# Optimization experiments

Measured on AMD Instinct MI355X. Metric: run time of the kernel, lower is better.

The kernel has to match this reference:

```python
import jax, jax.numpy as jnp
import numpy as np

# Model constants (match init_kwargs)
V_SIZE = 6144
D = 1024
K = 32            # SNN frames per token
N_LAYERS = 4
B = 2
S = 256
SUR_ALPHA = 4.0   # surrogate sigmoid alpha (dynamic _mpd_alpha affects grads only; fixed here)


def rmsnorm(x, w, eps=1e-6):
    return x * jax.lax.rsqrt(jnp.mean(x * x, axis=-1, keepdims=True) + eps) * w


def plif_scan(beta, u, v_th, alpha_sur):
    """PLIF row-param parallel scan: V[t] = beta*V[t-1] + u[t] (v_init = 0),
    spike[t] = Heaviside(V[t] - v_th) with sigmoid surrogate (straight-through).
    u: (T, B, D); beta, v_th: broadcastable to (B, D)."""
    A = jnp.broadcast_to(beta, u.shape)

    def comb(c1, c2):
        a1, b1 = c1
        a2, b2 = c2
        return a1 * a2, a2 * b1 + b2

    _, V = jax.lax.associative_scan(comb, (A, u))  # linear first-order recurrence
    vs = V - v_th
    sg = jax.nn.sigmoid(alpha_sur * vs)
    spike = jax.lax.stop_gradient((vs >= 0).astype(u.dtype) - sg) + sg
    return spike


def setup_inputs() -> dict:
    key = jax.random.key(0)
    ks = jax.random.split(key, 8)
    sc = 1.0 / np.sqrt(D)
    inp = {}
    inp["token_ids"] = jax.random.randint(ks[0], (B, S), 0, V_SIZE)
    inp["embed"] = jax.random.normal(ks[1], (V_SIZE, D), jnp.float32) * 0.02
    inp["W_in"] = jax.random.normal(ks[2], (N_LAYERS, D, D), jnp.float32) * sc
    inp["W_out"] = jax.random.normal(ks[3], (N_LAYERS, D, D), jnp.float32) * sc
    inp["layer_beta"] = jnp.full((N_LAYERS, D), 0.5, jnp.float32)  # tau=2 -> decay 0.5
    inp["layer_vth"] = jnp.full((N_LAYERS, D), 0.3, jnp.float32)
    inp["out_norm_w"] = jnp.ones((D,), jnp.float32)
    inp["out_beta"] = jnp.full((D,), 0.5, jnp.float32)
    inp["out_vth"] = jnp.full((D,), 0.3, jnp.float32)
    inp["out_alpha"] = jnp.ones((1,), jnp.float32)
    inp["decode_w"] = jax.random.normal(ks[4], (D, D), jnp.float32) * sc
    inp["decode_b"] = jnp.zeros((D,), jnp.float32)
    inp["li_norm_w"] = jnp.ones((D,), jnp.float32)
    return inp


def reference(token_ids, embed, W_in, W_out, layer_beta, layer_vth,
              out_norm_w, out_beta, out_vth, out_alpha,
              decode_w, decode_b, li_norm_w):
    b, s = token_ids.shape
    # encode: embed lookup, repeat each token K times -> (T=s*K, b, D)
    emb = embed[token_ids]                                   # (b, s, D)
    x = jnp.repeat(emb[:, :, None, :], K, axis=2)            # (b, s, K, D)
    x = x.reshape(b, s * K, D).transpose(1, 0, 2)            # (T, b, D)
    # SNN decoder layers (PLIF recurrence + residual projections)
    for i in range(N_LAYERS):
        u = jnp.einsum('tbd,de->tbe', x, W_in[i])
        spike = plif_scan(layer_beta[i], u, layer_vth[i], SUR_ALPHA)
        x = x + jnp.einsum('tbd,de->tbe', spike * layer_vth[i], W_out[i])
    # decode: RMSNorm -> output PLIF neuron parallel scan -> spike current
    h = rmsnorm(x, out_norm_w)
    spike = plif_scan(out_beta, out_alpha * h, out_vth, SUR_ALPHA)
    v_out = spike * out_vth                                  # spike_current_activation
    # K-frame aggregation: (T, b, D) -> (s, K, b, D) -> mean over K -> (b, s, D)
    decoded = v_out.reshape(s, K, b, D).mean(axis=1).transpose(1, 0, 2)
    h2 = decoded @ decode_w.T + decode_b                     # decode_proj
    h2 = rmsnorm(h2, li_norm_w)                              # LateralInhibition norm
    return h2 @ embed.T                                      # tied LM head -> (b, s, V)
```

## Files before the change

### kernel.cpp

```cpp
#include <hip/hip_runtime.h>

typedef __bf16 bf16x8 __attribute__((ext_vector_type(8)));
typedef __bf16 bf16x4 __attribute__((ext_vector_type(4)));
typedef __bf16 bf16x2 __attribute__((ext_vector_type(2)));
typedef float  f32x4  __attribute__((ext_vector_type(4)));

constexpr int Bc = 2, Sc = 256, Kc = 32, Tc = 8192, Dc = 1024, Vc = 6144, NLc = 4;
constexpr int NPANEL = (Tc * Bc) / 128;
constexpr int UTS = NLc * Dc;

__device__ __forceinline__ void gload16(const void* g, void* l) {
    __builtin_amdgcn_global_load_lds(
        (const __attribute__((address_space(1))) unsigned int*)g,
        (__attribute__((address_space(3))) unsigned int*)l,
        16, 0, 0);
}

__device__ __forceinline__ int xcd_swz(int lin, int nwg) {
    int q = nwg >> 3, r = nwg & 7;
    int x = lin & 7, o = lin >> 3;
    int base = (x < r) ? x * (q + 1) : r * (q + 1) + (x - r) * q;
    return base + o;
}

__device__ __forceinline__ bool gate_or(const int* f, int n, int p) {
    bool g = false;
    for (int j = 0; j < n; ++j) g = g || (f[j * NPANEL + p] != 0);
    return g;
}

template<int EPI, int BM, int BN>
__global__ __launch_bounds__(256)
void gemm_bt(const __bf16* __restrict__ A, const __bf16* __restrict__ BT,
             int M, int N, int Kd,
             float* __restrict__ Cout, __bf16* __restrict__ outb,
             const float* __restrict__ bias)
{
    constexpr int MI = BM / 32, NI = BN / 32;
    constexpr int CA = BM / 32, CB = BN / 32;
    __shared__ char lds[(BM + BN) * 128];
    char* As = lds;
    char* Bs = lds + BM * 128;
    const int tid  = threadIdx.x;
    const int lane = tid & 63;
    const int wid  = tid >> 6;
    const int wm   = wid & 1, wn = wid >> 1;

    const int nwg = gridDim.x * gridDim.y;
    const int lin = blockIdx.y * gridDim.x + blockIdx.x;
    const int swz = xcd_swz(lin, nwg);
    const int bn  = (swz % gridDim.x) * BN;
    const int bm  = (swz / gridDim.x) * BM;

    const __bf16* asrc[CA];
#pragma unroll
    for (int i = 0; i < CA; ++i) {
        int chunk = i * 256 + tid;
        int row = chunk >> 3, kc = chunk & 7;
        int kcs = kc ^ (row & 7);
        asrc[i] = A + (size_t)(bm + row) * Kd + kcs * 8;
    }
    const __bf16* bsrc[CB];
#pragma unroll
    for (int i = 0; i < CB; ++i) {
        int chunk = i * 256 + tid;
        int row = chunk >> 3, kc = chunk & 7;
        int kcs = kc ^ (row & 7);
        bsrc[i] = BT + (size_t)(bn + row) * Kd + kcs * 8;
    }

    f32x4 acc[MI][NI] = {};

    for (int kt = 0; kt < Kd; kt += 64) {
#pragma unroll
        for (int i = 0; i < CA; ++i)
            gload16(asrc[i] + kt, As + (i * 256 + tid) * 16);
#pragma unroll
        for (int i = 0; i < CB; ++i)
            gload16(bsrc[i] + kt, Bs + (i * 256 + tid) * 16);
        __syncthreads();
#pragma unroll
        for (int kk = 0; kk < 2; ++kk) {
            const int ko = kk * 64 + ((lane >> 4) << 4);
            bf16x8 af[MI], bfr[NI];
#pragma unroll
            for (int mi = 0; mi < MI; ++mi) {
                int row = wm * (BM / 2) + mi * 16 + (lane & 15);
                af[mi] = *(const bf16x8*)(As + row * 128 + (ko ^ ((row & 7) << 4)));
            }
#pragma unroll
            for (int ni = 0; ni < NI; ++ni) {
                int row = wn * (BN / 2) + ni * 16 + (lane & 15);
                bfr[ni] = *(const bf16x8*)(Bs + row * 128 + (ko ^ ((row & 7) << 4)));
            }
#pragma unroll
            for (int mi = 0; mi < MI; ++mi)
#pragma unroll
                for (int ni = 0; ni < NI; ++ni)
                    acc[mi][ni] = __builtin_amdgcn_mfma_f32_16x16x32_bf16(
                        af[mi], bfr[ni], acc[mi][ni], 0, 0, 0);
        }
        __syncthreads();
    }

    const int cc = lane & 15, cr = (lane >> 4) * 4;
#pragma unroll
    for (int mi = 0; mi < MI; ++mi) {
#pragma unroll
        for (int ni = 0; ni < NI; ++ni) {
            int gcol = bn + wn * (BN / 2) + ni * 16 + cc;
#pragma unroll
            for (int r = 0; r < 4; ++r) {
                int grow = bm + wm * (BM / 2) + mi * 16 + cr + r;
                size_t idx = (size_t)grow * N + gcol;
                float v = acc[mi][ni][r];
                if (EPI == 0)      Cout[idx] = v;
                else if (EPI == 2) Cout[idx] = v + bias[gcol];
                else               outb[idx] = (__bf16)v;
            }
        }
    }
}

__global__ __launch_bounds__(1024)
void fused_layer(const __bf16* __restrict__ utok, const float* __restrict__ Win,
                 const float* __restrict__ Wout, const float* __restrict__ beta,
                 const float* __restrict__ vth, const __bf16* __restrict__ dxR,
                 __bf16* __restrict__ dxW, int* __restrict__ flags_all, int l)
{
    const int e  = threadIdx.x;
    const int p  = blockIdx.x;
    const int t0 = p * 64;
    const float bet = beta[e], vt = vth[e];
    float a = bet, S = 1.0f;
#pragma unroll
    for (int i = 0; i < 5; ++i) { S = S * (1.0f + a); a = a * a; }
    int* flags_l = flags_all + l * NPANEL;

    __shared__ int fm;
    __shared__ __bf16 srow[Dc];
    if (e == 0) fm = 0;
    __syncthreads();

    const bool pd  = gate_or(flags_all, l, p);
    const bool pdw = (p > 0) && gate_or(flags_all, l, p - 1);

    auto ut = [&](int tk, int b) -> float {
        return (float)utok[((size_t)tk * Bc + b) * UTS + e];
    };
    auto du_at = [&](int t, int b) -> float {
        __syncthreads();
        srow[e] = dxR[((size_t)t * Bc + b) * Dc + e];
        __syncthreads();
        float acc = 0.f;
        for (int d = 0; d < Dc; ++d)
            acc = fmaf((float)srow[d], Win[(size_t)d * Dc + e], acc);
        return acc;
    };

    bool spike = false;
    for (int b = 0; b < Bc; ++b) {
        float V = 0.f;
        if (p > 0) {
            if (!pdw) {
                for (int ti = 0; ti < 2; ++ti)
                    V = fmaf(a, V, ut(2 * p - 2 + ti, b) * S);
            } else {
                for (int t = t0 - 64; t < t0; ++t)
                    V = fmaf(bet, V, ut(t >> 5, b) + du_at(t, b));
            }
        }
        if (!pd) {
            for (int ti = 0; ti < 2; ++ti) {
                const float u = ut(2 * p + ti, b);
                float V1 = fmaf(bet, V, u);
                V = fmaf(a, V, u * S);
                spike = spike || (fmaxf(V1, V) >= vt);
            }
        } else {
            for (int k = 0; k < 64; ++k) {
                const int t = t0 + k;
                V = fmaf(bet, V, ut(t >> 5, b) + du_at(t, b));
                spike = spike || (V >= vt);
            }
        }
    }
    if (__any(spike) && (e & 63) == 0) atomicOr(&fm, 1);
    __syncthreads();
    const bool f = (fm != 0);
    if (e == 0) flags_l[p] = f ? 1 : 0;
    if (!f) {
        if (pd) {
            for (int rr = 0; rr < 128; ++rr)
                dxW[(size_t)(t0 * Bc + rr) * Dc + e] =
                    dxR[(size_t)(t0 * Bc + rr) * Dc + e];
        }
        return;
    }

    const __bf16 vtb = (__bf16)vt, zb = (__bf16)0.f;
    for (int b = 0; b < Bc; ++b) {
        float V = 0.f;
        if (p > 0) {
            if (!pdw) {
                for (int ti = 0; ti < 2; ++ti)
                    V = fmaf(a, V, ut(2 * p - 2 + ti, b) * S);
            } else {
                for (int t = t0 - 64; t < t0; ++t)
                    V = fmaf(bet, V, ut(t >> 5, b) + du_at(t, b));
            }
        }
        for (int k = 0; k < 64; ++k) {
            const int t = t0 + k;
            float u = ut(t >> 5, b);
            if (pd) u += du_at(t, b);
            V = fmaf(bet, V, u);
            __syncthreads();
            srow[e] = (V >= vt) ? vtb : zb;
            __syncthreads();
            float acc2 = 0.f;
            for (int d = 0; d < Dc; ++d)
                acc2 = fmaf((float)srow[d], Wout[(size_t)d * Dc + e], acc2);
            size_t r = (size_t)t * Bc + b;
            float base = pd ? (float)dxR[r * Dc + e] : 0.f;
            dxW[r * Dc + e] = (__bf16)(base + acc2);
        }
    }
}

__global__ __launch_bounds__(256)
void out_scan2(const float* __restrict__ htok, const __bf16* __restrict__ dxf,
               const int* __restrict__ tok, const float* __restrict__ embed,
               const float* __restrict__ onw, const float* __restrict__ alpha_p,
               const float* __restrict__ obeta, const float* __restrict__ ovth,
               const int* __restrict__ flags, __bf16* __restrict__ decoded)
{
    const int tid = threadIdx.x;
    const int s = blockIdx.x, b = blockIdx.y;
    const float al = alpha_p[0];
    const f32x4 bet = ((const f32x4*)obeta)[tid];
    const f32x4 vt  = ((const f32x4*)ovth)[tid];
    f32x4 a = bet, S = {1.f, 1.f, 1.f, 1.f};
#pragma unroll
    for (int i = 0; i < 5; ++i) {
#pragma unroll
        for (int c = 0; c < 4; ++c) { S[c] *= 1.0f + a[c]; a[c] *= a[c]; }
    }

    const int t0 = s * Kc;
    const int tlo = (t0 >= 64) ? t0 - 64 : 0;
    bool dirty = false;
    for (int c = tlo >> 6; c <= (t0 + Kc - 1) >> 6; ++c)
        dirty = dirty || gate_or(flags, NLc, c);

    f32x4 V = {0,0,0,0}, sum = {0,0,0,0};
    if (!dirty) {
        for (int tk = (s >= 2 ? s - 2 : 0); tk < s; ++tk) {
            f32x4 h = ((const f32x4*)(htok + ((size_t)tk * Bc + b) * Dc))[tid];
#pragma unroll
            for (int c = 0; c < 4; ++c) V[c] = fmaf(a[c], V[c], al * h[c] * S[c]);
        }
        f32x4 h = ((const f32x4*)(htok + ((size_t)s * Bc + b) * Dc))[tid];
        for (int k = 0; k < Kc; ++k) {
#pragma unroll
            for (int c = 0; c < 4; ++c) {
                V[c] = fmaf(bet[c], V[c], al * h[c]);
                sum[c] += (V[c] >= vt[c]) ? vt[c] : 0.f;
            }
        }
    } else {
        const f32x4 wv = ((const f32x4*)onw)[tid];
        __shared__ float red[4];
        for (int t = tlo; t < t0 + Kc; ++t) {
            const bool g = gate_or(flags, NLc, t >> 6);
            f32x4 h;
            if (g) {
                size_t r = (size_t)t * Bc + b;
                int id = tok[b * Sc + (t >> 5)];
                f32x4 v = ((const f32x4*)(embed + (size_t)id * Dc))[tid];
                bf16x4 dv = ((const bf16x4*)(dxf + r * Dc))[tid];
#pragma unroll
                for (int c = 0; c < 4; ++c) v[c] += (float)dv[c];
                float ss = v[0]*v[0] + v[1]*v[1] + v[2]*v[2] + v[3]*v[3];
#pragma unroll
                for (int off = 32; off >= 1; off >>= 1) ss += __shfl_down(ss, off);
                if ((tid & 63) == 0) red[tid >> 6] = ss;
                __syncthreads();
                float tot = red[0] + red[1] + red[2] + red[3];
                __syncthreads();
                float sc = rsqrtf(tot * (1.0f / Dc) + 1e-6f);
#pragma unroll
                for (int c = 0; c < 4; ++c) h[c] = v[c] * sc * wv[c];
            } else {
                h = ((const f32x4*)(htok + ((size_t)(t >> 5) * Bc + b) * Dc))[tid];
            }
#pragma unroll
            for (int c = 0; c < 4; ++c) {
                V[c] = fmaf(bet[c], V[c], al * h[c]);
                if (t >= t0) sum[c] += (V[c] >= vt[c]) ? vt[c] : 0.f;
            }
        }
    }
    bf16x4 o;
#pragma unroll
    for (int c = 0; c < 4; ++c) o[c] = (__bf16)(sum[c] * (1.0f / 32.0f));
    ((bf16x4*)(decoded + ((size_t)b * Sc + s) * Dc))[tid] = o;
}

__global__ __launch_bounds__(256)
void prep(const float* __restrict__ W_in, const float* __restrict__ embed,
          const float* __restrict__ decode_w, const int* __restrict__ tok,
          const float* __restrict__ onw, __bf16* __restrict__ wT_in,
          __bf16* __restrict__ emb_bf, __bf16* __restrict__ decw_bf,
          __bf16* __restrict__ xtok, float* __restrict__ h_tok,
          int* __restrict__ flags)
{
    const int blk = blockIdx.x;
    const int tid = threadIdx.x;
    if (blk < 4096) {
        __shared__ float tile[32][33];
        const int mat = blk >> 10;
        const int t2  = blk & 1023;
        const int d0  = (t2 & 31) * 32, e0 = (t2 >> 5) * 32;
        const float* Wm = W_in + (size_t)mat * Dc * Dc;
        __bf16*      Wo = wT_in + (size_t)mat * Dc * Dc;
        const int tx = tid & 31, ty = tid >> 5;
#pragma unroll
        for (int i = 0; i < 4; ++i)
            tile[ty + i*8][tx] = Wm[(size_t)(d0 + ty + i*8) * Dc + e0 + tx];
        __syncthreads();
        const int txp = tid & 15, tyw = tid >> 4;
#pragma unroll
        for (int i = 0; i < 2; ++i) {
            int r = tyw + 16 * i;
            bf16x2 o;
            o[0] = (__bf16)tile[2*txp][r];
            o[1] = (__bf16)tile[2*txp + 1][r];
            *(bf16x2*)(&Wo[(size_t)(e0 + r) * Dc + d0 + 2*txp]) = o;
        }
    } else if (blk < 7680) {
        const float* src; __bf16* dst; int idx;
        if (blk < 7168) { src = embed;    dst = emb_bf;  idx = (blk - 4096) * 256 + tid; }
        else            { src = decode_w; dst = decw_bf; idx = (blk - 7168) * 256 + tid; }
        const f32x4* pp = (const f32x4*)src + (size_t)idx * 2;
        f32x4 v0 = pp[0], v1 = pp[1];
        bf16x8 o;
        o[0]=(__bf16)v0[0]; o[1]=(__bf16)v0[1]; o[2]=(__bf16)v0[2]; o[3]=(__bf16)v0[3];
        o[4]=(__bf16)v1[0]; o[5]=(__bf16)v1[1]; o[6]=(__bf16)v1[2]; o[7]=(__bf16)v1[3];
        ((bf16x8*)dst)[idx] = o;
    } else {
        const int r = blk - 7680;
        if (r == 0) { flags[tid] = 0; flags[tid + 256] = 0; }
        const int s = r >> 1, b = r & 1;
        const int id = tok[b * Sc + s];
        const f32x4 v = ((const f32x4*)(embed + (size_t)id * Dc))[tid];
        float ss = v[0]*v[0] + v[1]*v[1] + v[2]*v[2] + v[3]*v[3];
#pragma unroll
        for (int off = 32; off >= 1; off >>= 1) ss += __shfl_down(ss, off);
        __shared__ float red[4];
        if ((tid & 63) == 0) red[tid >> 6] = ss;
        __syncthreads();
        float tot = red[0] + red[1] + red[2] + red[3];
        float sc = rsqrtf(tot * (1.0f / Dc) + 1e-6f);
        const f32x4 wv = ((const f32x4*)onw)[tid];
        bf16x4 o; o[0]=(__bf16)v[0]; o[1]=(__bf16)v[1]; o[2]=(__bf16)v[2]; o[3]=(__bf16)v[3];
        ((bf16x4*)(xtok + (size_t)r * Dc))[tid] = o;
        f32x4 h = {v[0]*sc*wv[0], v[1]*sc*wv[1], v[2]*sc*wv[2], v[3]*sc*wv[3]};
        ((f32x4*)(h_tok + (size_t)r * Dc))[tid] = h;
    }
}

__global__ __launch_bounds__(256)
void rmsnorm_rows(const float* __restrict__ in, const float* __restrict__ w,
                  __bf16* __restrict__ outb)
{
    const int r = blockIdx.x;
    const int tid = threadIdx.x;
    const f32x4 v = ((const f32x4*)(in + (size_t)r * Dc))[tid];
    float ss = v[0]*v[0] + v[1]*v[1] + v[2]*v[2] + v[3]*v[3];
#pragma unroll
    for (int off = 32; off >= 1; off >>= 1) ss += __shfl_down(ss, off);
    __shared__ float red[4];
    if ((tid & 63) == 0) red[tid >> 6] = ss;
    __syncthreads();
    float tot = red[0] + red[1] + red[2] + red[3];
    float sc = rsqrtf(tot * (1.0f / Dc) + 1e-6f);
    const f32x4 wv = ((const f32x4*)w)[tid];
    bf16x4 o;
    o[0]=(__bf16)(v[0]*sc*wv[0]); o[1]=(__bf16)(v[1]*sc*wv[1]);
    o[2]=(__bf16)(v[2]*sc*wv[2]); o[3]=(__bf16)(v[3]*sc*wv[3]);
    ((bf16x4*)(outb + (size_t)r * Dc))[tid] = o;
}

extern "C" void kernel_launch(void* const* d_in, const int* in_sizes, int n_in,
                              void* d_out, int out_size, void* d_ws, size_t ws_size,
                              hipStream_t stream)
{
    const int*   token_ids  = (const int*)  d_in[0];
    const float* embed      = (const float*)d_in[1];
    const float* W_in       = (const float*)d_in[2];
    const float* W_out      = (const float*)d_in[3];
    const float* layer_beta = (const float*)d_in[4];
    const float* layer_vth  = (const float*)d_in[5];
    const float* out_norm_w = (const float*)d_in[6];
    const float* out_beta   = (const float*)d_in[7];
    const float* out_vth    = (const float*)d_in[8];
    const float* out_alpha  = (const float*)d_in[9];
    const float* decode_w   = (const float*)d_in[10];
    const float* decode_b   = (const float*)d_in[11];
    const float* li_norm_w  = (const float*)d_in[12];
    float* out = (float*)d_out;

    size_t off = 0;
    auto alloc = [&](size_t bytes) -> void* {
        void* p = (char*)d_ws + off;
        off += (bytes + 255) & ~(size_t)255;
        return p;
    };
    __bf16* dxA      = (__bf16*)alloc((size_t)Tc * Bc * Dc * 2);
    __bf16* dxB      = (__bf16*)alloc((size_t)Tc * Bc * Dc * 2);
    __bf16* u_tokall = (__bf16*)alloc((size_t)Bc * Sc * UTS * 2);
    float*  h_tok    = (float*) alloc((size_t)Bc * Sc * Dc * 4);
    __bf16* xtok     = (__bf16*)alloc((size_t)Bc * Sc * Dc * 2);
    __bf16* wT_in    = (__bf16*)alloc((size_t)NLc * Dc * Dc * 2);
    __bf16* emb_bf   = (__bf16*)alloc((size_t)Vc * Dc * 2);
    __bf16* decw_bf  = (__bf16*)alloc((size_t)Dc * Dc * 2);
    __bf16* decoded  = (__bf16*)alloc((size_t)Bc * Sc * Dc * 2);
    float*  h2       = (float*) alloc((size_t)Bc * Sc * Dc * 4);
    __bf16* h2n      = (__bf16*)alloc((size_t)Bc * Sc * Dc * 2);
    int*    flags    = (int*)   alloc((size_t)NLc * NPANEL * 4);
    __bf16* dxbuf[2] = { dxA, dxB };

    prep<<<8192, 256, 0, stream>>>(W_in, embed, decode_w, token_ids, out_norm_w,
                                   wT_in, emb_bf, decw_bf, xtok, h_tok, flags);

    gemm_bt<3, 64, 64><<<dim3(UTS / 64, (Bc * Sc) / 64), 256, 0, stream>>>(
        xtok, wT_in, Bc * Sc, UTS, Dc, nullptr, u_tokall, nullptr);

    for (int l = 0; l < NLc; ++l) {
        fused_layer<<<NPANEL, 1024, 0, stream>>>(
            u_tokall + (size_t)l * Dc, W_in + (size_t)l * Dc * Dc,
            W_out + (size_t)l * Dc * Dc, layer_beta + (size_t)l * Dc,
            layer_vth + (size_t)l * Dc, dxbuf[l & 1], dxbuf[(l + 1) & 1],
            flags, l);
    }
    __bf16* dxf = dxbuf[NLc & 1];

    out_scan2<<<dim3(Sc, Bc), 256, 0, stream>>>(
        h_tok, dxf, token_ids, embed, out_norm_w, out_alpha, out_beta, out_vth,
        flags, decoded);
    gemm_bt<2, 64, 64><<<dim3(Dc / 64, (Bc * Sc) / 64), 256, 0, stream>>>(
        decoded, decw_bf, Bc * Sc, Dc, Dc, h2, nullptr, decode_b);
    rmsnorm_rows<<<Bc * Sc, 256, 0, stream>>>(h2, li_norm_w, h2n);
    gemm_bt<0, 64, 128><<<dim3(Vc / 128, (Bc * Sc) / 64), 256, 0, stream>>>(
        h2n, emb_bf, Bc * Sc, Vc, Dc, out, nullptr, nullptr);
}
```

Baseline: 83.01 us.

## Speculatively detect spike-free layers in one kernel and early-exit layer kernels

Adds a spec_scan kernel that checks, for all four layers at once, whether any neuron in each panel would spike given token-constant inputs, and also computes the output scan and decoded tensor assuming no layer spikes. A global dirty flag is set if any panel spikes. The per-layer fused kernels and the output scan then return immediately when nothing is dirty, so most launches become near-empty. This relies on the data-dependent sparsity check and adds one extra kernel plus reads of the dirty flag.

After: 80.64 us. -2.8%, faster.

```diff
diff --git a/kernel.cpp b/kernel.cpp
--- a/kernel.cpp
+++ b/kernel.cpp
@@ -123,11 +123,101 @@
 }
 
 __global__ __launch_bounds__(1024)
+void spec_scan(const __bf16* __restrict__ utok_base,
+               const float* __restrict__ lbeta, const float* __restrict__ lvth,
+               const float* __restrict__ htok, const float* __restrict__ alpha_p,
+               const float* __restrict__ obeta, const float* __restrict__ ovth,
+               __bf16* __restrict__ decoded, int* __restrict__ flags,
+               int* __restrict__ dirtyAny)
+{
+    const int e = threadIdx.x;
+    const int p = blockIdx.x;
+    __shared__ int fm;
+    if (e == 0) fm = 0;
+    __syncthreads();
+
+    unsigned mybits = 0;
+#pragma unroll
+    for (int l = 0; l < NLc; ++l) {
+        const __bf16* utok = utok_base + (size_t)l * Dc;
+        const float bet = lbeta[l * Dc + e], vt = lvth[l * Dc + e];
+        float a = bet, S = 1.0f;
+#pragma unroll
+        for (int i = 0; i < 5; ++i) { S = S * (1.0f + a); a = a * a; }
+        bool spike = false;
+        for (int b = 0; b < Bc; ++b) {
+            float V = 0.f;
+            if (p > 0) {
+#pragma unroll
+                for (int ti = 0; ti < 2; ++ti) {
+                    float u = (float)utok[((size_t)(2 * p - 2 + ti) * Bc + b) * UTS + e];
+                    V = fmaf(a, V, u * S);
+                }
+            }
+#pragma unroll
+            for (int ti = 0; ti < 2; ++ti) {
+                float u = (float)utok[((size_t)(2 * p + ti) * Bc + b) * UTS + e];
+                float V1 = fmaf(bet, V, u);
+                V = fmaf(a, V, u * S);
+                spike = spike || (fmaxf(V1, V) >= vt);
+            }
+        }
+        if (spike) mybits |= 1u << l;
+    }
+    if (__any(mybits & 1) || __any(mybits & 2) || __any(mybits & 4) ||
+        __any(mybits & 8)) {
+        unsigned wor = 0;
+#pragma unroll
+        for (int l = 0; l < NLc; ++l)
+            if (__any(mybits & (1u << l))) wor |= 1u << l;
+        if ((e & 63) == 0 && wor) atomicOr(&fm, (int)wor);
+    }
+    __syncthreads();
+    const int f = fm;
+    if (e < NLc) flags[e * NPANEL + p] = (f >> e) & 1;
+    if (e == 0 && f) atomicOr(dirtyAny, 1);
+
+    const int w = e >> 6, lane = e & 63;
+    const int ridx = w & 3, cq = w >> 2;
+    const int s = 2 * p + (ridx >> 1), b = ridx & 1;
+    const int gi = lane + 64 * cq;
+    const float al = alpha_p[0];
+    const f32x4 obet = ((const f32x4*)obeta)[gi];
+    const f32x4 ovt  = ((const f32x4*)ovth)[gi];
+    f32x4 oa = obet, oS = {1.f, 1.f, 1.f, 1.f};
+#pragma unroll
+    for (int i = 0; i < 5; ++i) {
+#pragma unroll
+        for (int c = 0; c < 4; ++c) { oS[c] *= 1.0f + oa[c]; oa[c] *= oa[c]; }
+    }
+    f32x4 V = {0, 0, 0, 0}, sum = {0, 0, 0, 0};
+    for (int tk = (s >= 2 ? s - 2 : 0); tk < s; ++tk) {
+        f32x4 h = ((const f32x4*)(htok + ((size_t)tk * Bc + b) * Dc))[gi];
+#pragma unroll
+        for (int c = 0; c < 4; ++c) V[c] = fmaf(oa[c], V[c], al * h[c] * oS[c]);
+    }
+    f32x4 h = ((const f32x4*)(htok + ((size_t)s * Bc + b) * Dc))[gi];
+    for (int k = 0; k < Kc; ++k) {
+#pragma unroll
+        for (int c = 0; c < 4; ++c) {
+            V[c] = fmaf(obet[c], V[c], al * h[c]);
+            sum[c] += (V[c] >= ovt[c]) ? ovt[c] : 0.f;
+        }
+    }
+    bf16x4 o;
+#pragma unroll
+    for (int c = 0; c < 4; ++c) o[c] = (__bf16)(sum[c] * (1.0f / 32.0f));
+    ((bf16x4*)(decoded + ((size_t)b * Sc + s) * Dc))[gi] = o;
+}
+
+__global__ __launch_bounds__(1024)
 void fused_layer(const __bf16* __restrict__ utok, const float* __restrict__ Win,
                  const float* __restrict__ Wout, const float* __restrict__ beta,
                  const float* __restrict__ vth, const __bf16* __restrict__ dxR,
-                 __bf16* __restrict__ dxW, int* __restrict__ flags_all, int l)
-{
+                 __bf16* __restrict__ dxW, int* __restrict__ flags_all, int l,
+                 const int* __restrict__ dirty)
+{
+    if (dirty[0] == 0) return;
     const int e  = threadIdx.x;
     const int p  = blockIdx.x;
     const int t0 = p * 64;
@@ -233,8 +323,10 @@
                const int* __restrict__ tok, const float* __restrict__ embed,
                const float* __restrict__ onw, const float* __restrict__ alpha_p,
                const float* __restrict__ obeta, const float* __restrict__ ovth,
-               const int* __restrict__ flags, __bf16* __restrict__ decoded)
-{
+               const int* __restrict__ flags, __bf16* __restrict__ decoded,
+               const int* __restrict__ dirtyp)
+{
+    if (dirtyp[0] == 0) return;
     const int tid = threadIdx.x;
     const int s = blockIdx.x, b = blockIdx.y;
     const float al = alpha_p[0];
@@ -350,7 +442,10 @@
         ((bf16x8*)dst)[idx] = o;
     } else {
         const int r = blk - 7680;
-        if (r == 0) { flags[tid] = 0; flags[tid + 256] = 0; }
+        if (r == 0) {
+            flags[tid] = 0; flags[tid + 256] = 0;
+            if (tid == 0) flags[512] = 0;
+        }
         const int s = r >> 1, b = r & 1;
         const int id = tok[b * Sc + s];
         const f32x4 v = ((const f32x4*)(embed + (size_t)id * Dc))[tid];
@@ -427,8 +522,9 @@
     __bf16* decw_bf  = (__bf16*)alloc((size_t)Dc * Dc * 2);
     __bf16* decoded  = (__bf16*)alloc((size_t)Bc * Sc * Dc * 2);
     float*  h2       = (float*) alloc((size_t)Bc * Sc * Dc * 4);
-    __bf16* h2n      = (__bf16*)alloc((size_t)Bc * Sc * Dc * 2);
-    int*    flags    = (int*)   alloc((size_t)NLc * NPANEL * 4);
+    __bf16* h2n     = (__bf16*)alloc((size_t)Bc * Sc * Dc * 2);
+    int*    flags    = (int*)   alloc(((size_t)NLc * NPANEL + 64) * 4);
+    int*    dirtyAny = flags + NLc * NPANEL;
     __bf16* dxbuf[2] = { dxA, dxB };
 
     prep<<<8192, 256, 0, stream>>>(W_in, embed, decode_w, token_ids, out_norm_w,
@@ -436,19 +532,23 @@
 
     gemm_bt<3, 64, 64><<<dim3(UTS / 64, (Bc * Sc) / 64), 256, 0, stream>>>(
         xtok, wT_in, Bc * Sc, UTS, Dc, nullptr, u_tokall, nullptr);
+
+    spec_scan<<<NPANEL, 1024, 0, stream>>>(
+        u_tokall, layer_beta, layer_vth, h_tok, out_alpha, out_beta, out_vth,
+        decoded, flags, dirtyAny);
 
     for (int l = 0; l < NLc; ++l) {
         fused_layer<<<NPANEL, 1024, 0, stream>>>(
             u_tokall + (size_t)l * Dc, W_in + (size_t)l * Dc * Dc,
             W_out + (size_t)l * Dc * Dc, layer_beta + (size_t)l * Dc,
             layer_vth + (size_t)l * Dc, dxbuf[l & 1], dxbuf[(l + 1) & 1],
-            flags, l);
+            flags, l, dirtyAny);
     }
     __bf16* dxf = dxbuf[NLc & 1];
-
     out_scan2<<<dim3(Sc, Bc), 256, 0, stream>>>(
         h_tok, dxf, token_ids, embed, out_norm_w, out_alpha, out_beta, out_vth,
-        flags, decoded);
+        flags, decoded, dirtyAny);
+
     gemm_bt<2, 64, 64><<<dim3(Dc / 64, (Bc * Sc) / 64), 256, 0, stream>>>(
         decoded, decw_bf, Bc * Sc, Dc, Dc, h2, nullptr, decode_b);
     rmsnorm_rows<<<Bc * Sc, 256, 0, stream>>>(h2, li_norm_w, h2n);
```
